# Optimization experiments

Measured on AMD Instinct MI355X. Metric: run time of the kernel, lower is better.

## Reference

```python
import jax, jax.numpy as jnp
import numpy as np

TOPK_FRAC = 0.05
TOPK_MIN = 5
TOPK_MAX = 64


def setup_inputs() -> dict:
    key = jax.random.key(0)
    ks = jax.random.split(key, 8)
    N, H, B = 131072, 256, 512
    x = jax.random.normal(ks[0], (N, H), dtype=jnp.float32)
    batch = jnp.sort(jax.random.randint(ks[1], (N,), 0, B, dtype=jnp.int32))
    W1 = jax.random.normal(ks[2], (H, H // 2), dtype=jnp.float32) * 0.05
    b1 = jax.random.normal(ks[3], (H // 2,), dtype=jnp.float32) * 0.05
    W2 = jax.random.normal(ks[4], (H // 2, 1), dtype=jnp.float32) * 0.05
    b2 = jax.random.normal(ks[5], (1,), dtype=jnp.float32) * 0.05
    Wf = jax.random.normal(ks[6], (4 * H, H), dtype=jnp.float32) * 0.05
    bf = jax.random.normal(ks[7], (H,), dtype=jnp.float32) * 0.05
    return {"x": x, "batch": batch, "W1": W1, "b1": b1, "W2": W2,
            "b2": b2, "Wf": Wf, "bf": bf, "num_graphs": B}


def _forward(x, batch, W1, b1, W2, b2, Wf, bf, B):
    N = x.shape[0]
    # attention scores per node: MLP -> scalar
    s = (jax.nn.relu(x @ W1 + b1) @ W2 + b2)[:, 0]  # [N]
    # pyg_softmax: segment-wise stable softmax over nodes of each graph
    seg_max = jax.ops.segment_max(s, batch, num_segments=B)
    seg_max = jnp.where(jnp.isfinite(seg_max), seg_max, 0.0)  # guard empty segs
    e = jnp.exp(s - seg_max[batch])
    denom = jax.ops.segment_sum(e, batch, num_segments=B)
    w = e / denom[batch]                                    # [N]
    # pools
    x_attn = jax.ops.segment_sum(x * w[:, None], batch, num_segments=B)
    counts = jax.ops.segment_sum(jnp.ones((N,), jnp.int32), batch, num_segments=B)
    cnt_f = jnp.maximum(counts, 1).astype(x.dtype)
    x_mean = jax.ops.segment_sum(x, batch, num_segments=B) / cnt_f[:, None]
    x_max = jax.ops.segment_max(x, batch, num_segments=B)
    x_max = jnp.where(counts[:, None] > 0, x_max, 0.0)
    # per-graph dynamic k
    n = counts
    k = jnp.maximum(TOPK_MIN, jnp.ceil(TOPK_FRAC * n.astype(jnp.float32)).astype(jnp.int32))
    k = jnp.minimum(jnp.minimum(k, TOPK_MAX), n)            # [B]
    # fused segment top-k mean: sort nodes by (batch asc, w desc), keep rank<k
    order = jnp.lexsort((-w, batch))
    starts = jnp.concatenate([jnp.zeros((1,), jnp.int32), jnp.cumsum(counts)[:-1].astype(jnp.int32)])
    bs = batch[order]
    rank = jnp.arange(N, dtype=jnp.int32) - starts[bs]
    sel = (rank < k[bs]).astype(x.dtype)
    x_topk = jax.ops.segment_sum(x[order] * sel[:, None], bs, num_segments=B)
    x_topk = x_topk / jnp.maximum(k, 1).astype(x.dtype)[:, None]
    g = jax.nn.relu(jnp.concatenate([x_mean, x_attn, x_max, x_topk], axis=1) @ Wf + bf)
    return g


def reference(x, batch, W1, b1, W2, b2, Wf, bf, num_graphs):
    return _forward(x, batch, W1, b1, W2, b2, Wf, bf, num_graphs)
```

## Files before the change

kernel.cpp:

```cpp
#include <hip/hip_runtime.h>
#include <math.h>

#define H 256
#define HH 128
#define B_GRAPHS 512

typedef __attribute__((ext_vector_type(8))) short bfrag8;
typedef __attribute__((ext_vector_type(16))) float f32x16;

__global__ void k_prep_w1(const float* __restrict__ W1, ushort* __restrict__ W1b) {
  const int idx = blockIdx.x * 256 + threadIdx.x;
  const int k = idx >> 7, c = idx & 127;
  const float v = W1[idx];
  const uint u = __builtin_bit_cast(uint, v);
  const float r = v - __builtin_bit_cast(float, u & 0xFFFF0000u);
  const int base = (((k >> 4) * 2 + ((k >> 3) & 1)) * 128 + c) * 8 + (k & 7);
  W1b[base] = (ushort)(u >> 16);
  W1b[32768 + base] = (ushort)(__builtin_bit_cast(uint, r) >> 16);
}

__global__ void k_seg_bounds(const int* __restrict__ batch, int* __restrict__ seg_start,
                             int N, int B) {
  int b = blockIdx.x * blockDim.x + threadIdx.x;
  if (b > B) return;
  int lo = 0, hi = N;
  while (lo < hi) {
    int mid = (lo + hi) >> 1;
    if (batch[mid] < b) lo = mid + 1; else hi = mid;
  }
  seg_start[b] = lo;
}

__device__ __forceinline__ void splitbf(const float4 v0, const float4 v1,
                                        bfrag8& a0, bfrag8& a1) {
  const float vals[8] = {v0.x, v0.y, v0.z, v0.w, v1.x, v1.y, v1.z, v1.w};
#pragma unroll
  for (int e = 0; e < 8; ++e) {
    const uint u = __builtin_bit_cast(uint, vals[e]);
    a0[e] = (short)(u >> 16);
    const float r = vals[e] - __builtin_bit_cast(float, u & 0xFFFF0000u);
    a1[e] = (short)(__builtin_bit_cast(uint, r) >> 16);
  }
}

__global__ __launch_bounds__(256, 3) void k_score_mfma(
    const float* __restrict__ x, const ushort* __restrict__ W1b,
    const float* __restrict__ b1, const float* __restrict__ W2,
    const float* __restrict__ b2, float* __restrict__ s_out) {
  __shared__ float part[4][16][128];
  const int t = threadIdx.x;
  const int lane = t & 63;
  const int w = t >> 6;
  const int nl = lane & 31, g = lane >> 5;
  const int node0 = blockIdx.x * 32;

  f32x16 acc[4];
  acc[0] = (f32x16)0.f; acc[1] = (f32x16)0.f;
  acc[2] = (f32x16)0.f; acc[3] = (f32x16)0.f;

  const float* gsrc = x + (size_t)(node0 + nl) * H + w * 64 + g * 8;
  float4 xv[4][2];
#pragma unroll
  for (int sub = 0; sub < 4; ++sub) {
    xv[sub][0] = *(const float4*)(gsrc + sub * 16);
    xv[sub][1] = *(const float4*)(gsrc + sub * 16 + 4);
  }

#pragma unroll
  for (int sub = 0; sub < 4; ++sub) {
    const int kks = w * 4 + sub;
    bfrag8 a0, a1;
    splitbf(xv[sub][0], xv[sub][1], a0, a1);
#pragma unroll
    for (int j = 0; j < 4; ++j) {
      const ushort* bp = W1b + (size_t)((kks * 2 + g) * 128 + j * 32 + nl) * 8;
      const bfrag8 b0 = *(const bfrag8*)bp;
      const bfrag8 b1f = *(const bfrag8*)(bp + 32768);
      acc[j] = __builtin_amdgcn_mfma_f32_32x32x16_bf16(a0, b0, acc[j], 0, 0, 0);
      acc[j] = __builtin_amdgcn_mfma_f32_32x32x16_bf16(a0, b1f, acc[j], 0, 0, 0);
      acc[j] = __builtin_amdgcn_mfma_f32_32x32x16_bf16(a1, b0, acc[j], 0, 0, 0);
    }
  }

  const float b2v = b2[0];
  const int hb = (t & 15) * 8;
  const int nloc = t >> 4;
  float b1q[8], w2q[8];
#pragma unroll
  for (int e = 0; e < 8; ++e) {
    b1q[e] = b1[hb + e];
    w2q[e] = W2[hb + e];
  }

#pragma unroll
  for (int P = 0; P < 2; ++P) {
#pragma unroll
    for (int j = 0; j < 4; ++j)
#pragma unroll
      for (int rr = 0; rr < 8; ++rr) {
        const int nd = (rr & 3) + 8 * (rr >> 2) + 4 * g;
        part[w][nd][j * 32 + nl] = acc[j][P * 8 + rr];
      }
    __syncthreads();
    float h8[8];
#pragma unroll
    for (int e = 0; e < 8; e += 4) {
      const float4 s0 = *(const float4*)&part[0][nloc][hb + e];
      const float4 s1 = *(const float4*)&part[1][nloc][hb + e];
      const float4 s2 = *(const float4*)&part[2][nloc][hb + e];
      const float4 s3 = *(const float4*)&part[3][nloc][hb + e];
      h8[e + 0] = s0.x + s1.x + s2.x + s3.x;
      h8[e + 1] = s0.y + s1.y + s2.y + s3.y;
      h8[e + 2] = s0.z + s1.z + s2.z + s3.z;
      h8[e + 3] = s0.w + s1.w + s2.w + s3.w;
    }
    float v = 0.f;
#pragma unroll
    for (int e = 0; e < 8; ++e)
      v = fmaf(fmaxf(h8[e] + b1q[e], 0.f), w2q[e], v);
#pragma unroll
    for (int m = 1; m < 16; m <<= 1) v += __shfl_xor(v, m);
    if ((t & 15) == 0) s_out[node0 + P * 16 + nloc] = v + b2v;
    if (P == 0) __syncthreads();
  }
}

__global__ __launch_bounds__(512) void k_pool_fused(const float* __restrict__ x,
                                                    const float* __restrict__ s,
                                                    const int* __restrict__ seg_start,
                                                    float* __restrict__ pooled) {
  const int b = blockIdx.x;
  const int t = threadIdx.x;
  const int start = seg_start[b];
  const int end = seg_start[b + 1];
  const int n = end - start;

  __shared__ float s_lds[1024];
  __shared__ float red[512];
  __shared__ float thr_sh;
  __shared__ int thri_sh;
  __shared__ float r4[8][264];

  const bool fits = (n <= 1024);
  if (fits) {
    for (int i = t; i < n; i += 512) s_lds[i] = s[start + i];
  }
  __syncthreads();
  const float* sseg = fits ? s_lds : (s + start);

  float m = -INFINITY;
  for (int i = t; i < n; i += 512) m = fmaxf(m, sseg[i]);
  red[t] = m;
  __syncthreads();
  for (int off = 256; off > 0; off >>= 1) {
    if (t < off) red[t] = fmaxf(red[t], red[t + off]);
    __syncthreads();
  }
  const float smax = red[0];
  __syncthreads();
  float d = 0.f;
  for (int i = t; i < n; i += 512) d += __expf(sseg[i] - smax);
  red[t] = d;
  __syncthreads();
  for (int off = 256; off > 0; off >>= 1) {
    if (t < off) red[t] += red[t + off];
    __syncthreads();
  }
  const float denom = red[0];
  __syncthreads();
  const float inv_denom = (denom > 0.f) ? 1.f / denom : 0.f;

  int k = 0;
  if (n > 0) {
    k = (int)ceilf(0.05f * (float)n);
    if (k < 5) k = 5;
    if (k > 64) k = 64;
    if (k > n) k = n;
  }

  if (t < 64) {
    float pk = INFINITY;
    int pidx = -1;
    for (int r = 0; r < k; ++r) {
      float bk = -INFINITY;
      int bi = 0x7fffffff;
      for (int i = t; i < n; i += 64) {
        const float si = sseg[i];
        const int gi = start + i;
        const bool below = (si < pk) || (si == pk && gi > pidx);
        if (below && (si > bk || (si == bk && gi < bi))) { bk = si; bi = gi; }
      }
#pragma unroll
      for (int off = 32; off > 0; off >>= 1) {
        const float ok = __shfl_xor(bk, off);
        const int oi = __shfl_xor(bi, off);
        if (ok > bk || (ok == bk && oi < bi)) { bk = ok; bi = oi; }
      }
      pk = bk;
      pidx = bi;
    }
    if (t == 0) {
      thr_sh = (k > 0) ? pk : INFINITY;
      thri_sh = (k > 0) ? pidx : -1;
    }
  }
  __syncthreads();
  const float thr = thr_sh;
  const int thri = thri_sh;

  const int fq = t & 63;
  const int sub = t >> 6;
  float mean[4] = {0.f, 0.f, 0.f, 0.f};
  float attn[4] = {0.f, 0.f, 0.f, 0.f};
  float tk[4] = {0.f, 0.f, 0.f, 0.f};
  float mx[4] = {-INFINITY, -INFINITY, -INFINITY, -INFINITY};
  for (int i = sub; i < n; i += 8) {
    const float si = sseg[i];
    const float wi = __expf(si - smax);
    const int gi = start + i;
    const bool sel = (si > thr) || (si == thr && gi <= thri);
    const float4 xv = *reinterpret_cast<const float4*>(x + (size_t)gi * H + fq * 4);
    mean[0] += xv.x; mean[1] += xv.y; mean[2] += xv.z; mean[3] += xv.w;
    attn[0] = fmaf(xv.x, wi, attn[0]);
    attn[1] = fmaf(xv.y, wi, attn[1]);
    attn[2] = fmaf(xv.z, wi, attn[2]);
    attn[3] = fmaf(xv.w, wi, attn[3]);
    mx[0] = fmaxf(mx[0], xv.x);
    mx[1] = fmaxf(mx[1], xv.y);
    mx[2] = fmaxf(mx[2], xv.z);
    mx[3] = fmaxf(mx[3], xv.w);
    if (sel) {
      tk[0] += xv.x; tk[1] += xv.y; tk[2] += xv.z; tk[3] += xv.w;
    }
  }
  float* po = pooled + (size_t)b * 1024;
  const float invn = 1.f / (float)(n > 0 ? n : 1);
  const float invk = (k > 0) ? 1.f / (float)k : 0.f;
  *reinterpret_cast<float4*>(&r4[sub][fq * 4]) = make_float4(mean[0], mean[1], mean[2], mean[3]);
  __syncthreads();
  if (t < 256) {
    float tot = 0.f;
#pragma unroll
    for (int q = 0; q < 8; ++q) tot += r4[q][t];
    po[t] = tot * invn;
  }
  __syncthreads();
  *reinterpret_cast<float4*>(&r4[sub][fq * 4]) = make_float4(attn[0], attn[1], attn[2], attn[3]);
  __syncthreads();
  if (t < 256) {
    float tot = 0.f;
#pragma unroll
    for (int q = 0; q < 8; ++q) tot += r4[q][t];
    po[256 + t] = tot * inv_denom;
  }
  __syncthreads();
  *reinterpret_cast<float4*>(&r4[sub][fq * 4]) = make_float4(mx[0], mx[1], mx[2], mx[3]);
  __syncthreads();
  if (t < 256) {
    float tot = -INFINITY;
#pragma unroll
    for (int q = 0; q < 8; ++q) tot = fmaxf(tot, r4[q][t]);
    po[512 + t] = (n > 0) ? tot : 0.f;
  }
  __syncthreads();
  *reinterpret_cast<float4*>(&r4[sub][fq * 4]) = make_float4(tk[0], tk[1], tk[2], tk[3]);
  __syncthreads();
  if (t < 256) {
    float tot = 0.f;
#pragma unroll
    for (int q = 0; q < 8; ++q) tot += r4[q][t];
    po[768 + t] = tot * invk;
  }
}

__global__ __launch_bounds__(256) void k_gemm(const float* __restrict__ pooled,
                                              const float* __restrict__ Wf,
                                              float* __restrict__ gacc) {
  const int t = threadIdx.x;
  const int r0 = blockIdx.x * 8;
  const int kc0 = blockIdx.y * 128;
  __shared__ float ps[8][132];
  {
    const int r = t >> 5;
    const int c = (t & 31) << 2;
    *reinterpret_cast<float4*>(&ps[r][c]) =
        *reinterpret_cast<const float4*>(pooled + (size_t)(r0 + r) * 1024 + kc0 + c);
  }
  __syncthreads();
  float acc[8];
#pragma unroll
  for (int r = 0; r < 8; ++r) acc[r] = 0.f;
#pragma unroll 4
  for (int c = 0; c < 128; ++c) {
    const float wf = Wf[(size_t)(kc0 + c) * 256 + t];
#pragma unroll
    for (int r = 0; r < 8; ++r) acc[r] = fmaf(ps[r][c], wf, acc[r]);
  }
  float* go = gacc + ((size_t)blockIdx.y * B_GRAPHS + r0) * 256;
#pragma unroll
  for (int r = 0; r < 8; ++r) go[r * 256 + t] = acc[r];
}

__global__ __launch_bounds__(256) void k_out(const float* __restrict__ gacc,
                                             const float* __restrict__ bf,
                                             float* __restrict__ out) {
  const int i = blockIdx.x * 256 + threadIdx.x;
  float v = bf[i & 255];
#pragma unroll
  for (int ks = 0; ks < 8; ++ks) v += gacc[(size_t)ks * (B_GRAPHS * 256) + i];
  out[i] = fmaxf(v, 0.f);
}

extern "C" void kernel_launch(void* const* d_in, const int* in_sizes, int n_in,
                              void* d_out, int out_size, void* d_ws, size_t ws_size,
                              hipStream_t stream) {
  const float* x  = (const float*)d_in[0];
  const int* batch = (const int*)d_in[1];
  const float* W1 = (const float*)d_in[2];
  const float* b1 = (const float*)d_in[3];
  const float* W2 = (const float*)d_in[4];
  const float* b2 = (const float*)d_in[5];
  const float* Wf = (const float*)d_in[6];
  const float* bf = (const float*)d_in[7];
  const int N = in_sizes[1];
  const int B = B_GRAPHS;

  float* ws = (float*)d_ws;
  float* s = ws;
  int* seg_start = (int*)(ws + N);
  float* pooled = ws + N + 1024;
  float* gacc = pooled + (size_t)B * 1024;
  ushort* W1b = (ushort*)(gacc + (size_t)8 * B * 256);

  k_prep_w1<<<dim3(128), dim3(256), 0, stream>>>(W1, W1b);
  k_seg_bounds<<<dim3((B + 1 + 255) / 256), dim3(256), 0, stream>>>(batch, seg_start, N, B);
  k_score_mfma<<<dim3(N / 32), dim3(256), 0, stream>>>(x, W1b, b1, W2, b2, s);
  k_pool_fused<<<dim3(B), dim3(512), 0, stream>>>(x, s, seg_start, pooled);
  k_gemm<<<dim3(B / 8, 8), dim3(256), 0, stream>>>(pooled, Wf, gacc);
  k_out<<<dim3((B * 256) / 256), dim3(256), 0, stream>>>(gacc, bf, (float*)d_out);
}
```

Measured before the change: 111.0 us.

## Split score GEMM over output columns per wave instead of K-split

The score kernel now stages the x tile into LDS as split bf16 hi/lo halves with coalesced loads. Each wave then computes a distinct 32-column slice of the hidden layer over the full K=256, which removes the cross-wave partial-sum reduction through LDS. Two independent accumulators break the MFMA dependency chain, and occupancy is raised to 4 blocks per SM. In exchange it adds an LDS round trip for the A operand and an extra barrier.

```diff
diff --git a/kernel.cpp b/kernel.cpp
--- a/kernel.cpp
+++ b/kernel.cpp
@@ -31,97 +31,78 @@
   seg_start[b] = lo;
 }
 
-__device__ __forceinline__ void splitbf(const float4 v0, const float4 v1,
-                                        bfrag8& a0, bfrag8& a1) {
-  const float vals[8] = {v0.x, v0.y, v0.z, v0.w, v1.x, v1.y, v1.z, v1.w};
-#pragma unroll
-  for (int e = 0; e < 8; ++e) {
-    const uint u = __builtin_bit_cast(uint, vals[e]);
-    a0[e] = (short)(u >> 16);
-    const float r = vals[e] - __builtin_bit_cast(float, u & 0xFFFF0000u);
-    a1[e] = (short)(__builtin_bit_cast(uint, r) >> 16);
-  }
-}
-
-__global__ __launch_bounds__(256, 3) void k_score_mfma(
+__global__ __launch_bounds__(256, 4) void k_score_mfma(
     const float* __restrict__ x, const ushort* __restrict__ W1b,
     const float* __restrict__ b1, const float* __restrict__ W2,
     const float* __restrict__ b2, float* __restrict__ s_out) {
-  __shared__ float part[4][16][128];
+  __shared__ ushort ash[2][32][260];
   const int t = threadIdx.x;
   const int lane = t & 63;
   const int w = t >> 6;
   const int nl = lane & 31, g = lane >> 5;
   const int node0 = blockIdx.x * 32;
 
-  f32x16 acc[4];
-  acc[0] = (f32x16)0.f; acc[1] = (f32x16)0.f;
-  acc[2] = (f32x16)0.f; acc[3] = (f32x16)0.f;
-
-  const float* gsrc = x + (size_t)(node0 + nl) * H + w * 64 + g * 8;
-  float4 xv[4][2];
-#pragma unroll
-  for (int sub = 0; sub < 4; ++sub) {
-    xv[sub][0] = *(const float4*)(gsrc + sub * 16);
-    xv[sub][1] = *(const float4*)(gsrc + sub * 16 + 4);
-  }
-
-#pragma unroll
-  for (int sub = 0; sub < 4; ++sub) {
-    const int kks = w * 4 + sub;
-    bfrag8 a0, a1;
-    splitbf(xv[sub][0], xv[sub][1], a0, a1);
-#pragma unroll
-    for (int j = 0; j < 4; ++j) {
-      const ushort* bp = W1b + (size_t)((kks * 2 + g) * 128 + j * 32 + nl) * 8;
-      const bfrag8 b0 = *(const bfrag8*)bp;
-      const bfrag8 b1f = *(const bfrag8*)(bp + 32768);
-      acc[j] = __builtin_amdgcn_mfma_f32_32x32x16_bf16(a0, b0, acc[j], 0, 0, 0);
-      acc[j] = __builtin_amdgcn_mfma_f32_32x32x16_bf16(a0, b1f, acc[j], 0, 0, 0);
-      acc[j] = __builtin_amdgcn_mfma_f32_32x32x16_bf16(a1, b0, acc[j], 0, 0, 0);
-    }
-  }
-
-  const float b2v = b2[0];
-  const int hb = (t & 15) * 8;
-  const int nloc = t >> 4;
-  float b1q[8], w2q[8];
-#pragma unroll
-  for (int e = 0; e < 8; ++e) {
-    b1q[e] = b1[hb + e];
-    w2q[e] = W2[hb + e];
-  }
-
-#pragma unroll
-  for (int P = 0; P < 2; ++P) {
-#pragma unroll
-    for (int j = 0; j < 4; ++j)
-#pragma unroll
-      for (int rr = 0; rr < 8; ++rr) {
-        const int nd = (rr & 3) + 8 * (rr >> 2) + 4 * g;
-        part[w][nd][j * 32 + nl] = acc[j][P * 8 + rr];
+  {
+    const float* base = x + (size_t)node0 * H + w * 2048 + lane * 4;
+    float4 v[8];
+#pragma unroll
+    for (int i = 0; i < 8; ++i) v[i] = *(const float4*)(base + i * 256);
+#pragma unroll
+    for (int i = 0; i < 8; ++i) {
+      const int r = w * 8 + i;
+      const float vals[4] = {v[i].x, v[i].y, v[i].z, v[i].w};
+      ushort m[4], rr[4];
+#pragma unroll
+      for (int e = 0; e < 4; ++e) {
+        const uint u = __builtin_bit_cast(uint, vals[e]);
+        m[e] = (ushort)(u >> 16);
+        const float res = vals[e] - __builtin_bit_cast(float, u & 0xFFFF0000u);
+        rr[e] = (ushort)(__builtin_bit_cast(uint, res) >> 16);
       }
-    __syncthreads();
-    float h8[8];
-#pragma unroll
-    for (int e = 0; e < 8; e += 4) {
-      const float4 s0 = *(const float4*)&part[0][nloc][hb + e];
-      const float4 s1 = *(const float4*)&part[1][nloc][hb + e];
-      const float4 s2 = *(const float4*)&part[2][nloc][hb + e];
-      const float4 s3 = *(const float4*)&part[3][nloc][hb + e];
-      h8[e + 0] = s0.x + s1.x + s2.x + s3.x;
-      h8[e + 1] = s0.y + s1.y + s2.y + s3.y;
-      h8[e + 2] = s0.z + s1.z + s2.z + s3.z;
-      h8[e + 3] = s0.w + s1.w + s2.w + s3.w;
-    }
+      *(uint2*)&ash[0][r][lane * 4] =
+          make_uint2((uint)m[0] | ((uint)m[1] << 16), (uint)m[2] | ((uint)m[3] << 16));
+      *(uint2*)&ash[1][r][lane * 4] =
+          make_uint2((uint)rr[0] | ((uint)rr[1] << 16), (uint)rr[2] | ((uint)rr[3] << 16));
+    }
+  }
+  __syncthreads();
+
+  f32x16 acc[2];
+  acc[0] = (f32x16)0.f;
+  acc[1] = (f32x16)0.f;
+  const ushort* bbase = W1b + (size_t)(w * 32 + nl) * 8 + (size_t)g * 1024;
+
+#pragma unroll
+  for (int kks = 0; kks < 16; ++kks) {
+    const bfrag8 a0 = *(const bfrag8*)&ash[0][nl][kks * 16 + g * 8];
+    const bfrag8 a1 = *(const bfrag8*)&ash[1][nl][kks * 16 + g * 8];
+    const bfrag8 b0 = *(const bfrag8*)(bbase + kks * 2048);
+    const bfrag8 b1f = *(const bfrag8*)(bbase + kks * 2048 + 32768);
+    acc[0] = __builtin_amdgcn_mfma_f32_32x32x16_bf16(a0, b0, acc[0], 0, 0, 0);
+    acc[1] = __builtin_amdgcn_mfma_f32_32x32x16_bf16(a0, b1f, acc[1], 0, 0, 0);
+    acc[0] = __builtin_amdgcn_mfma_f32_32x32x16_bf16(a1, b0, acc[0], 0, 0, 0);
+  }
+
+  __syncthreads();
+  float* part = (float*)ash;
+#pragma unroll
+  for (int r = 0; r < 16; ++r) {
+    const int row = (r & 3) + 8 * (r >> 2) + 4 * g;
+    part[row * 132 + w * 32 + nl] = acc[0][r] + acc[1][r];
+  }
+  __syncthreads();
+  {
+    const int node = t >> 3, seg = t & 7;
     float v = 0.f;
 #pragma unroll
-    for (int e = 0; e < 8; ++e)
-      v = fmaf(fmaxf(h8[e] + b1q[e], 0.f), w2q[e], v);
-#pragma unroll
-    for (int m = 1; m < 16; m <<= 1) v += __shfl_xor(v, m);
-    if ((t & 15) == 0) s_out[node0 + P * 16 + nloc] = v + b2v;
-    if (P == 0) __syncthreads();
+    for (int e = 0; e < 16; ++e) {
+      const int hcol = seg * 16 + e;
+      const float hv = part[node * 132 + hcol] + b1[hcol];
+      v = fmaf(fmaxf(hv, 0.f), W2[hcol], v);
+    }
+#pragma unroll
+    for (int m = 1; m <= 4; m <<= 1) v += __shfl_xor(v, m);
+    if ((t & 7) == 0) s_out[node0 + node] = v + b2[0];
   }
 }
 
```

Result: no change. 112.6 us (+1.5%).
